# Performance work log

Hardware: AMD Instinct MI355X
Metric: run time of the kernel (lower is better)

The kernel has to match this reference:

```python
import jax, jax.numpy as jnp
import numpy as np
import math

EMBED_DIM = 1024
NUM_HEADS = 16
HEAD_DIM = EMBED_DIM // NUM_HEADS


def setup_inputs() -> dict:
    key = jax.random.key(0)
    ks = jax.random.split(key, 5)
    x = jax.random.normal(ks[0], (4, 2048, EMBED_DIM), dtype=jnp.float32)
    # Linear params (torch nn.Linear: y = x @ W.T + b); init scale ~ 1/sqrt(fan_in)
    s = 1.0 / math.sqrt(EMBED_DIM)
    qkv_w = jax.random.uniform(ks[1], (3 * EMBED_DIM, EMBED_DIM), jnp.float32, -s, s)
    qkv_b = jax.random.uniform(ks[2], (3 * EMBED_DIM,), jnp.float32, -s, s)
    proj_w = jax.random.uniform(ks[3], (EMBED_DIM, EMBED_DIM), jnp.float32, -s, s)
    proj_b = jax.random.uniform(ks[4], (EMBED_DIM,), jnp.float32, -s, s)
    return {"x": x, "qkv_w": qkv_w, "qkv_b": qkv_b, "proj_w": proj_w, "proj_b": proj_b}


def reference(x, qkv_w, qkv_b, proj_w, proj_b):
    bsz, num_tokens, dim = x.shape
    qkv = x @ qkv_w.T + qkv_b  # [B, S, 3*D]
    qkv = qkv.reshape(bsz, num_tokens, 3, NUM_HEADS, HEAD_DIM)
    qkv = jnp.transpose(qkv, (2, 0, 3, 1, 4))  # [3, B, H, S, hd]
    q, k, v = qkv[0], qkv[1], qkv[2]
    scale = 1.0 / math.sqrt(HEAD_DIM)
    attn_scores = jnp.einsum('bhqd,bhkd->bhqk', q, k) * scale  # [B, H, S, S]
    attn = jax.nn.softmax(attn_scores, axis=-1)
    out = jnp.einsum('bhqk,bhkd->bhqd', attn, v)  # [B, H, S, hd]
    out = jnp.transpose(out, (0, 2, 1, 3)).reshape(bsz, num_tokens, dim)
    out = out @ proj_w.T + proj_b
    return out
```

## Files before the change

### kernel.cpp

```cpp
#include <hip/hip_runtime.h>
#include <stdint.h>

#define DEVICE static __device__ __forceinline__

typedef __bf16 bf16x8 __attribute__((ext_vector_type(8)));
typedef float f32x4 __attribute__((ext_vector_type(4)));

#define AS1 __attribute__((address_space(1)))
#define AS3 __attribute__((address_space(3)))

DEVICE void g2l16(const void* gptr, void* lptr) {
  __builtin_amdgcn_global_load_lds((AS1 uint32_t*)(uintptr_t)gptr,
                                   (AS3 uint32_t*)(uint32_t)(uintptr_t)lptr,
                                   16, 0, 0);
}

DEVICE float b2f(ushort h) {
  union { uint32_t u; float f; } v;
  v.u = ((uint32_t)h) << 16;
  return v.f;
}
DEVICE ushort f2b(float f) {
  union { float f; uint32_t u; } v;
  v.f = f;
  uint32_t u = v.u;
  return (ushort)((u + 0x7FFFu + ((u >> 16) & 1u)) >> 16);
}

#if defined(__has_builtin) && __has_builtin(__builtin_amdgcn_exp2f)
DEVICE float fast_exp2(float x) { return __builtin_amdgcn_exp2f(x); }
#else
extern "C" __device__ float __ocml_native_exp2_f32(float);
DEVICE float fast_exp2(float x) { return __ocml_native_exp2_f32(x); }
#endif

#define QSCALE 0.1803368801111244f

DEVICE int kperm(int x) {
  return (x & 0x23) | ((x & 0x18) >> 1) | ((x & 0x4) << 2);
}

__global__ void detect_dtype(const ushort* __restrict__ xu, int* __restrict__ flag) {
  __shared__ int bad;
  if (threadIdx.x == 0) bad = 0;
  __syncthreads();
  int mybad = 0;
#pragma unroll
  for (int j = 0; j < 8; ++j) {
    const int i = threadIdx.x * 8 + j;
    const ushort u = xu[2 * i];
    const int e = (u >> 7) & 0xFF;
    if (!(e == 0 || (e >= 96 && e <= 160))) mybad++;
  }
  atomicAdd(&bad, mybad);
  __syncthreads();
  if (threadIdx.x == 0) *flag = (bad > 512) ? 1 : 0;
}

__global__ void convert_all(const void* __restrict__ s0, const void* __restrict__ s1,
                            const void* __restrict__ s2, const void* __restrict__ s3,
                            const void* __restrict__ s4,
                            ushort* __restrict__ d0, ushort* __restrict__ d1,
                            ushort* __restrict__ d2, ushort* __restrict__ d3,
                            ushort* __restrict__ d4,
                            const int* __restrict__ flag) {
  const bool isf32 = (*flag != 0);
  for (int g = blockIdx.x * blockDim.x + threadIdx.x; g < 1573376;
       g += gridDim.x * blockDim.x) {
    const void* src; ushort* dst; int i;
    if (g < 1048576)      { src = s0; dst = d0; i = g; }
    else if (g < 1441792) { src = s1; dst = d1; i = g - 1048576; }
    else if (g < 1442176) { src = s2; dst = d2; i = g - 1441792; }
    else if (g < 1573248) { src = s3; dst = d3; i = g - 1442176; }
    else                  { src = s4; dst = d4; i = g - 1573248; }
    ushort pk[8];
    if (isf32) {
      const float4 a = ((const float4*)src)[2 * i];
      const float4 b = ((const float4*)src)[2 * i + 1];
      pk[0] = f2b(a.x); pk[1] = f2b(a.y); pk[2] = f2b(a.z); pk[3] = f2b(a.w);
      pk[4] = f2b(b.x); pk[5] = f2b(b.y); pk[6] = f2b(b.z); pk[7] = f2b(b.w);
      *(uint4*)&dst[8 * i] = *(const uint4*)pk;
    } else {
      *(uint4*)&dst[8 * i] = ((const uint4*)src)[i];
    }
  }
}

template <int MODE, int GN>
__global__ __launch_bounds__(512, 2)
void gemm256(const ushort* __restrict__ A, const ushort* __restrict__ W,
             const ushort* __restrict__ bias, ushort* __restrict__ O0,
             ushort* __restrict__ O1, ushort* __restrict__ O2,
             int M, int N, int K, const int* __restrict__ flag)
{
  __shared__ __align__(16) char smem[98304];

  const int tid = threadIdx.x;
  const int lane = tid & 63;
  const int wave = tid >> 6;
  const int quad = lane >> 4;
  const int lo = lane & 15;

  const int lin = blockIdx.y * gridDim.x + blockIdx.x;
  const int per = GN * gridDim.y;
  const int grp = lin / per;
  const int w   = lin % per;
  const int bxn = grp * GN + (w % GN);
  const int bym = w / GN;
  const int m0 = bym * 128;
  const int n0 = bxn * 256;

  const int wm = (wave >> 2) * 64;
  const int wn = (wave & 3) * 64;

  const int rA = tid >> 2;
  const int gA = (tid & 3) << 3;
  const size_t offA  = (size_t)(m0 + rA) * K + gA;
  const size_t offB0 = (size_t)(n0 + rA) * K + gA;
  const size_t offB1 = (size_t)(n0 + 128 + rA) * K + gA;
  const int dA = wave << 10;
  const int NT = K >> 5;

  f32x4 acc[4][4] = {};

#pragma unroll
  for (int t = 0; t < 2; ++t) {
    char* buf = smem + t * 24576;
    g2l16(A + offA  + t * 32, buf + dA);
    g2l16(W + offB0 + t * 32, buf + 8192 + dA);
    g2l16(W + offB1 + t * 32, buf + 16384 + dA);
  }
  asm volatile("s_waitcnt vmcnt(3)" ::: "memory");
  __builtin_amdgcn_s_barrier();

  for (int kt = 0; kt < NT; ++kt) {
    const char* buf = smem + (kt & 3) * 24576;
    const ushort* Al = (const ushort*)buf;
    const ushort* Bl = (const ushort*)(buf + 8192);
    const bool pf = (kt + 2 < NT);
    char* nbuf = smem + ((kt + 2) & 3) * 24576;

    if (pf) {
      g2l16(A + offA  + (size_t)(kt + 2) * 32, nbuf + dA);
      g2l16(W + offB0 + (size_t)(kt + 2) * 32, nbuf + 8192 + dA);
    }
    bf16x8 bfr[4], af[2];
#pragma unroll
    for (int nt = 0; nt < 4; ++nt)
      bfr[nt] = *(const bf16x8*)&Bl[(wn + nt * 16 + lo) * 32 + quad * 8];
#pragma unroll
    for (int mt = 0; mt < 2; ++mt)
      af[mt] = *(const bf16x8*)&Al[(wm + mt * 16 + lo) * 32 + quad * 8];
    __builtin_amdgcn_s_setprio(1);
#pragma unroll
    for (int mt = 0; mt < 2; ++mt)
#pragma unroll
      for (int nt = 0; nt < 4; ++nt)
        acc[mt][nt] = __builtin_amdgcn_mfma_f32_16x16x32_bf16(
            af[mt], bfr[nt], acc[mt][nt], 0, 0, 0);
    __builtin_amdgcn_s_setprio(0);
    __builtin_amdgcn_s_barrier();

    if (pf)
      g2l16(W + offB1 + (size_t)(kt + 2) * 32, nbuf + 16384 + dA);
    bf16x8 af2[2];
#pragma unroll
    for (int mt = 0; mt < 2; ++mt)
      af2[mt] = *(const bf16x8*)&Al[(wm + (mt + 2) * 16 + lo) * 32 + quad * 8];
    __builtin_amdgcn_s_setprio(1);
#pragma unroll
    for (int mt = 0; mt < 2; ++mt)
#pragma unroll
      for (int nt = 0; nt < 4; ++nt)
        acc[mt + 2][nt] = __builtin_amdgcn_mfma_f32_16x16x32_bf16(
            af2[mt], bfr[nt], acc[mt + 2][nt], 0, 0, 0);
    __builtin_amdgcn_s_setprio(0);

    if (kt < NT - 1) {
      if (pf) asm volatile("s_waitcnt vmcnt(3)" ::: "memory");
      else    asm volatile("s_waitcnt vmcnt(0)" ::: "memory");
      __builtin_amdgcn_s_barrier();
    }
  }

  if (MODE == 0) {
    const int which = n0 >> 10;
    if (which == 2) {
#pragma unroll
      for (int nt = 0; nt < 4; ++nt) {
        const int n = n0 + wn + nt * 16 + lo;
        const float bv = b2f(bias[n]);
        const int h = (n >> 6) & 15;
        const int d = n & 63;
#pragma unroll
        for (int mt = 0; mt < 4; ++mt) {
          const int m = m0 + wm + mt * 16 + quad * 4;
          const int b = m >> 11, s0 = m & 2047;
          ushort pk[4];
#pragma unroll
          for (int r = 0; r < 4; ++r) pk[r] = f2b(acc[mt][nt][r] + bv);
          *(uint2*)&O2[((size_t)(b * 16 + h) * 64 + d) * 2048 + s0] =
              *(const uint2*)pk;
        }
      }
    } else {
      const float qs = (which == 0) ? QSCALE : 1.0f;
      ushort* __restrict__ dst = (which == 0) ? O0 : O1;
      const int h = ((n0 + wn) >> 6) & 15;
      __syncthreads();
      ushort* scr = (ushort*)(smem + wave * 12288);
      float bv[4];
#pragma unroll
      for (int nt = 0; nt < 4; ++nt) bv[nt] = b2f(bias[n0 + wn + nt * 16 + lo]);
#pragma unroll
      for (int c2 = 0; c2 < 2; ++c2) {
#pragma unroll
        for (int mtl = 0; mtl < 2; ++mtl)
#pragma unroll
          for (int nt = 0; nt < 4; ++nt)
#pragma unroll
            for (int r = 0; r < 4; ++r)
              scr[(mtl * 16 + quad * 4 + r) * 88 + nt * 16 + lo] =
                  f2b((acc[c2 * 2 + mtl][nt][r] + bv[nt]) * qs);
        asm volatile("s_waitcnt lgkmcnt(0)" ::: "memory");
#pragma unroll
        for (int i = 0; i < 4; ++i) {
          const int id = lane + 64 * i;
          const int rowl = id >> 3, nch = id & 7;
          const uint4 val = *(const uint4*)&scr[rowl * 88 + nch * 8];
          const int m = m0 + wm + c2 * 32 + rowl;
          const int b = m >> 11;
          int s = m & 2047;
          if (which == 1) s = (s & ~63) | kperm(s & 63);
          *(uint4*)&dst[((size_t)(b * 16 + h) * 2048 + s) * 64 + nch * 8] = val;
        }
      }
    }
  } else {
    const bool f32out = (*flag != 0);
    float* Of = (float*)O0;
#pragma unroll
    for (int nt = 0; nt < 4; ++nt) {
      const int n = n0 + wn + nt * 16 + lo;
      const float bv = b2f(bias[n]);
#pragma unroll
      for (int mt = 0; mt < 4; ++mt)
#pragma unroll
        for (int r = 0; r < 4; ++r) {
          const int m = m0 + wm + mt * 16 + quad * 4 + r;
          const float val = acc[mt][nt][r] + bv;
          if (f32out) Of[(size_t)m * N + n] = val;
          else        O0[(size_t)m * N + n] = f2b(val);
        }
    }
  }
}

__global__ __launch_bounds__(256, 4)
void attn_fwd(const ushort* __restrict__ qp, const ushort* __restrict__ kp,
              const ushort* __restrict__ vp, ushort* __restrict__ o)
{
  __shared__ ushort Qs[128 * 64];
  __shared__ ushort Ks[64 * 64];
  __shared__ ushort Vt[64 * 64];

  const int tid = threadIdx.x;
  const int lane = tid & 63;
  const int wave = tid >> 6;
  const int quad = lane >> 4;
  const int lo = lane & 15;
  const int sw = (lo & 7) << 3;

  const int lin = blockIdx.y * gridDim.x + blockIdx.x;
  const int bh = (lin & 7) * 8 + ((lin >> 3) & 7);
  const int q0 = (lin >> 6) * 128;

  const ushort* Qg = qp + (size_t)bh * 2048 * 64;
  const ushort* Kg = kp + (size_t)bh * 2048 * 64;
  const ushort* Vg = vp + (size_t)bh * 64 * 2048;

#pragma unroll
  for (int i = 0; i < 4; ++i) {
    const int c = tid + 256 * i;
    const int row = c >> 3;
    const int kc = ((c ^ row) & 7) << 3;
    g2l16(Qg + (size_t)(q0 + row) * 64 + kc,
          (char*)Qs + ((wave << 6) + (i << 8)) * 16);
  }
  __syncthreads();

  bf16x8 qf[2][2];
#pragma unroll
  for (int mt = 0; mt < 2; ++mt)
#pragma unroll
    for (int ks = 0; ks < 2; ++ks)
      qf[mt][ks] = *(const bf16x8*)&Qs[(wave * 32 + mt * 16 + lo) * 64 +
                                       ((ks * 32 + quad * 8) ^ sw)];

  bf16x8 ones;
#pragma unroll
  for (int j = 0; j < 8; ++j) ones[j] = (__bf16)1.0f;

  f32x4 oacc[2][4] = {};
  f32x4 sumacc[2] = {};

  for (int j0 = 0; j0 < 2048; j0 += 64) {
    __syncthreads();
#pragma unroll
    for (int i = 0; i < 2; ++i) {
      const int c = tid + 256 * i;
      const int row = c >> 3;
      const int kc = ((c ^ row) & 7) << 3;
      g2l16(Kg + (size_t)(j0 + row) * 64 + kc,
            (char*)Ks + ((wave << 6) + (i << 8)) * 16);
      g2l16(Vg + (size_t)row * 2048 + j0 + kc,
            (char*)Vt + ((wave << 6) + (i << 8)) * 16);
    }
    __syncthreads();

    f32x4 sacc[2][4] = {};
#pragma unroll
    for (int ks = 0; ks < 2; ++ks) {
#pragma unroll
      for (int nt = 0; nt < 4; ++nt) {
        const bf16x8 kf =
            *(const bf16x8*)&Ks[(nt * 16 + lo) * 64 + ((ks * 32 + quad * 8) ^ sw)];
#pragma unroll
        for (int mt = 0; mt < 2; ++mt)
          sacc[mt][nt] = __builtin_amdgcn_mfma_f32_16x16x32_bf16(
              kf, qf[mt][ks], sacc[mt][nt], 0, 0, 0);
      }
    }

    bf16x8 pfr[2][2];
#pragma unroll
    for (int mt = 0; mt < 2; ++mt) {
      float p[4][4];
#pragma unroll
      for (int nt = 0; nt < 4; ++nt)
#pragma unroll
        for (int r = 0; r < 4; ++r)
          p[nt][r] = fast_exp2(sacc[mt][nt][r]);
#pragma unroll
      for (int b = 0; b < 2; ++b)
#pragma unroll
        for (int h = 0; h < 2; ++h)
#pragma unroll
          for (int r = 0; r < 4; ++r)
            pfr[mt][b][4 * h + r] = (__bf16)p[2 * b + h][r];
    }

#pragma unroll
    for (int b = 0; b < 2; ++b) {
#pragma unroll
      for (int mt = 0; mt < 2; ++mt)
        sumacc[mt] = __builtin_amdgcn_mfma_f32_16x16x32_bf16(
            pfr[mt][b], ones, sumacc[mt], 0, 0, 0);
#pragma unroll
      for (int dt = 0; dt < 4; ++dt) {
        const bf16x8 vf =
            *(const bf16x8*)&Vt[(dt * 16 + lo) * 64 + ((b * 32 + quad * 8) ^ sw)];
#pragma unroll
        for (int mt = 0; mt < 2; ++mt)
          oacc[mt][dt] = __builtin_amdgcn_mfma_f32_16x16x32_bf16(
              pfr[mt][b], vf, oacc[mt][dt], 0, 0, 0);
      }
    }
  }

  const int b_ = bh >> 4;
  const int h = bh & 15;
#pragma unroll
  for (int mt = 0; mt < 2; ++mt) {
#pragma unroll
    for (int r = 0; r < 4; ++r) {
      const float inv = 1.0f / sumacc[mt][r];
      const int srow = q0 + wave * 32 + mt * 16 + quad * 4 + r;
#pragma unroll
      for (int dt = 0; dt < 4; ++dt) {
        o[(((size_t)(b_ * 2048 + srow)) << 10) + h * 64 + dt * 16 + lo] =
            f2b(oacc[mt][dt][r] * inv);
      }
    }
  }
}

extern "C" void kernel_launch(void* const* d_in, const int* in_sizes, int n_in,
                              void* d_out, int out_size, void* d_ws, size_t ws_size,
                              hipStream_t stream) {
  const size_t N_X  = (size_t)4 * 2048 * 1024;
  const size_t N_WQ = (size_t)3072 * 1024;
  const size_t N_BQ = 3072;
  const size_t N_WP = (size_t)1024 * 1024;
  const size_t N_BP = 1024;
  const size_t HSD  = (size_t)64 * 2048 * 64;

  ushort* xb = (ushort*)d_ws;
  ushort* wq = xb + N_X;
  ushort* bq = wq + N_WQ;
  ushort* wp = bq + N_BQ;
  ushort* bp = wp + N_WP;
  ushort* qb = bp + N_BP;
  ushort* kb = qb + HSD;
  ushort* vb = kb + HSD;
  ushort* ab = vb + HSD;
  int* flag  = (int*)(ab + HSD);

  detect_dtype<<<1, 256, 0, stream>>>((const ushort*)d_in[0], flag);
  convert_all<<<2048, 256, 0, stream>>>(d_in[0], d_in[1], d_in[2], d_in[3], d_in[4],
                                        xb, wq, bq, wp, bp, flag);

  gemm256<0, 4><<<dim3(12, 64), dim3(512), 0, stream>>>(
      xb, wq, bq, qb, kb, vb, 8192, 3072, 1024, flag);
  attn_fwd<<<dim3(16, 64), dim3(256), 0, stream>>>(qb, kb, vb, ab);
  gemm256<1, 4><<<dim3(4, 64), dim3(512), 0, stream>>>(
      ab, wp, bp, (ushort*)d_out, nullptr, nullptr, 8192, 1024, 1024, flag);
}
```

Baseline: 262.1 us.

## Enlarge GEMM tile to 256x256 with K=64 steps and swizzled LDS

The GEMM block tile grows from 128x256 to 256x256, with each wave computing 128x64. The K step doubles to 64 and uses an XOR-swizzled LDS layout, and the four-stage pipeline becomes a two-stage double buffer of 64 KB halves. The goal is more reuse per loaded byte, fewer bank conflicts and fewer iterations. The cost is twice the LDS (128 KB, so likely one block per CU), more accumulator registers, extra barriers inside each K step, and half as many blocks, which lowers occupancy and can leave CUs idle in the last wave of blocks.

After: 268.7 us. +2.5%, slower.

```diff
diff --git a/kernel.cpp b/kernel.cpp
--- a/kernel.cpp
+++ b/kernel.cpp
@@ -93,13 +93,14 @@
              ushort* __restrict__ O1, ushort* __restrict__ O2,
              int M, int N, int K, const int* __restrict__ flag)
 {
-  __shared__ __align__(16) char smem[98304];
+  __shared__ __align__(16) char smem[131072];
 
   const int tid = threadIdx.x;
   const int lane = tid & 63;
   const int wave = tid >> 6;
   const int quad = lane >> 4;
   const int lo = lane & 15;
+  const int swk = lo & 7;
 
   const int lin = blockIdx.y * gridDim.x + blockIdx.x;
   const int per = GN * gridDim.y;
@@ -107,78 +108,83 @@
   const int w   = lin % per;
   const int bxn = grp * GN + (w % GN);
   const int bym = w / GN;
-  const int m0 = bym * 128;
+  const int m0 = bym * 256;
   const int n0 = bxn * 256;
 
-  const int wm = (wave >> 2) * 64;
+  const int wm = (wave >> 2) * 128;
   const int wn = (wave & 3) * 64;
 
-  const int rA = tid >> 2;
-  const int gA = (tid & 3) << 3;
-  const size_t offA  = (size_t)(m0 + rA) * K + gA;
-  const size_t offB0 = (size_t)(n0 + rA) * K + gA;
-  const size_t offB1 = (size_t)(n0 + 128 + rA) * K + gA;
-  const int dA = wave << 10;
-  const int NT = K >> 5;
-
-  f32x4 acc[4][4] = {};
-
-#pragma unroll
-  for (int t = 0; t < 2; ++t) {
-    char* buf = smem + t * 24576;
-    g2l16(A + offA  + t * 32, buf + dA);
-    g2l16(W + offB0 + t * 32, buf + 8192 + dA);
-    g2l16(W + offB1 + t * 32, buf + 16384 + dA);
-  }
-  asm volatile("s_waitcnt vmcnt(3)" ::: "memory");
+  const int koffE = ((tid ^ (tid >> 3)) & 7) << 3;
+  const int r0 = tid >> 3;
+  const size_t offA = (size_t)(m0 + r0) * K + koffE;
+  const size_t offB = (size_t)(n0 + r0) * K + koffE;
+  const int NT = K >> 6;
+
+  f32x4 acc[8][4] = {};
+
+#pragma unroll
+  for (int i = 0; i < 4; ++i) {
+    g2l16(A + offA + (size_t)(64 * i) * K, smem + (wave << 10) + (i << 13));
+    g2l16(W + offB + (size_t)(64 * i) * K, smem + 32768 + (wave << 10) + (i << 13));
+  }
+  asm volatile("s_waitcnt vmcnt(0)" ::: "memory");
   __builtin_amdgcn_s_barrier();
 
   for (int kt = 0; kt < NT; ++kt) {
-    const char* buf = smem + (kt & 3) * 24576;
+    char* buf  = smem + (kt & 1) * 65536;
+    char* nbuf = smem + ((kt + 1) & 1) * 65536;
     const ushort* Al = (const ushort*)buf;
-    const ushort* Bl = (const ushort*)(buf + 8192);
-    const bool pf = (kt + 2 < NT);
-    char* nbuf = smem + ((kt + 2) & 3) * 24576;
-
+    const ushort* Bl = (const ushort*)(buf + 32768);
+    const bool pf = (kt + 1 < NT);
+    const size_t nk = (size_t)(kt + 1) << 6;
+
+    bf16x8 bfr[4][2];
+#pragma unroll
+    for (int p = 0; p < 4; ++p) {
+      if (p == 0 && pf) {
+#pragma unroll
+        for (int i = 0; i < 4; ++i)
+          g2l16(A + offA + (size_t)(64 * i) * K + nk,
+                nbuf + (wave << 10) + (i << 13));
+      }
+      if (p == 1 && pf) {
+#pragma unroll
+        for (int i = 0; i < 4; ++i)
+          g2l16(W + offB + (size_t)(64 * i) * K + nk,
+                nbuf + 32768 + (wave << 10) + (i << 13));
+      }
+      if (p == 0) {
+#pragma unroll
+        for (int nt = 0; nt < 4; ++nt)
+#pragma unroll
+          for (int ks = 0; ks < 2; ++ks)
+            bfr[nt][ks] = *(const bf16x8*)&Bl[(wn + nt * 16 + lo) * 64 +
+                                              (((ks * 4 + quad) ^ swk) << 3)];
+      }
+      bf16x8 af[2][2];
+#pragma unroll
+      for (int mt2 = 0; mt2 < 2; ++mt2)
+#pragma unroll
+        for (int ks = 0; ks < 2; ++ks)
+          af[mt2][ks] = *(const bf16x8*)&Al[(wm + (2 * p + mt2) * 16 + lo) * 64 +
+                                            (((ks * 4 + quad) ^ swk) << 3)];
+      __builtin_amdgcn_s_barrier();
+      asm volatile("s_waitcnt lgkmcnt(0)" ::: "memory");
+      __builtin_amdgcn_sched_barrier(0);
+      __builtin_amdgcn_s_setprio(1);
+#pragma unroll
+      for (int mt2 = 0; mt2 < 2; ++mt2)
+#pragma unroll
+        for (int nt = 0; nt < 4; ++nt)
+#pragma unroll
+          for (int ks = 0; ks < 2; ++ks)
+            acc[2 * p + mt2][nt] = __builtin_amdgcn_mfma_f32_16x16x32_bf16(
+                af[mt2][ks], bfr[nt][ks], acc[2 * p + mt2][nt], 0, 0, 0);
+      __builtin_amdgcn_s_setprio(0);
+      __builtin_amdgcn_s_barrier();
+    }
     if (pf) {
-      g2l16(A + offA  + (size_t)(kt + 2) * 32, nbuf + dA);
-      g2l16(W + offB0 + (size_t)(kt + 2) * 32, nbuf + 8192 + dA);
-    }
-    bf16x8 bfr[4], af[2];
-#pragma unroll
-    for (int nt = 0; nt < 4; ++nt)
-      bfr[nt] = *(const bf16x8*)&Bl[(wn + nt * 16 + lo) * 32 + quad * 8];
-#pragma unroll
-    for (int mt = 0; mt < 2; ++mt)
-      af[mt] = *(const bf16x8*)&Al[(wm + mt * 16 + lo) * 32 + quad * 8];
-    __builtin_amdgcn_s_setprio(1);
-#pragma unroll
-    for (int mt = 0; mt < 2; ++mt)
-#pragma unroll
-      for (int nt = 0; nt < 4; ++nt)
-        acc[mt][nt] = __builtin_amdgcn_mfma_f32_16x16x32_bf16(
-            af[mt], bfr[nt], acc[mt][nt], 0, 0, 0);
-    __builtin_amdgcn_s_setprio(0);
-    __builtin_amdgcn_s_barrier();
-
-    if (pf)
-      g2l16(W + offB1 + (size_t)(kt + 2) * 32, nbuf + 16384 + dA);
-    bf16x8 af2[2];
-#pragma unroll
-    for (int mt = 0; mt < 2; ++mt)
-      af2[mt] = *(const bf16x8*)&Al[(wm + (mt + 2) * 16 + lo) * 32 + quad * 8];
-    __builtin_amdgcn_s_setprio(1);
-#pragma unroll
-    for (int mt = 0; mt < 2; ++mt)
-#pragma unroll
-      for (int nt = 0; nt < 4; ++nt)
-        acc[mt + 2][nt] = __builtin_amdgcn_mfma_f32_16x16x32_bf16(
-            af2[mt], bfr[nt], acc[mt + 2][nt], 0, 0, 0);
-    __builtin_amdgcn_s_setprio(0);
-
-    if (kt < NT - 1) {
-      if (pf) asm volatile("s_waitcnt vmcnt(3)" ::: "memory");
-      else    asm volatile("s_waitcnt vmcnt(0)" ::: "memory");
+      asm volatile("s_waitcnt vmcnt(0)" ::: "memory");
       __builtin_amdgcn_s_barrier();
     }
   }
@@ -193,7 +199,7 @@
         const int h = (n >> 6) & 15;
         const int d = n & 63;
 #pragma unroll
-        for (int mt = 0; mt < 4; ++mt) {
+        for (int mt = 0; mt < 8; ++mt) {
           const int m = m0 + wm + mt * 16 + quad * 4;
           const int b = m >> 11, s0 = m & 2047;
           ushort pk[4];
@@ -213,7 +219,7 @@
 #pragma unroll
       for (int nt = 0; nt < 4; ++nt) bv[nt] = b2f(bias[n0 + wn + nt * 16 + lo]);
 #pragma unroll
-      for (int c2 = 0; c2 < 2; ++c2) {
+      for (int c2 = 0; c2 < 4; ++c2) {
 #pragma unroll
         for (int mtl = 0; mtl < 2; ++mtl)
 #pragma unroll
@@ -244,7 +250,7 @@
       const int n = n0 + wn + nt * 16 + lo;
       const float bv = b2f(bias[n]);
 #pragma unroll
-      for (int mt = 0; mt < 4; ++mt)
+      for (int mt = 0; mt < 8; ++mt)
 #pragma unroll
         for (int r = 0; r < 4; ++r) {
           const int m = m0 + wm + mt * 16 + quad * 4 + r;
@@ -410,9 +416,9 @@
   convert_all<<<2048, 256, 0, stream>>>(d_in[0], d_in[1], d_in[2], d_in[3], d_in[4],
                                         xb, wq, bq, wp, bp, flag);
 
-  gemm256<0, 4><<<dim3(12, 64), dim3(512), 0, stream>>>(
+  gemm256<0, 4><<<dim3(12, 32), dim3(512), 0, stream>>>(
       xb, wq, bq, qb, kb, vb, 8192, 3072, 1024, flag);
   attn_fwd<<<dim3(16, 64), dim3(256), 0, stream>>>(qb, kb, vb, ab);
-  gemm256<1, 4><<<dim3(4, 64), dim3(512), 0, stream>>>(
+  gemm256<1, 4><<<dim3(4, 32), dim3(512), 0, stream>>>(
       ab, wp, bp, (ushort*)d_out, nullptr, nullptr, 8192, 1024, 1024, flag);
 }
```
